# Kernel tuning notes

Hardware: AMD Instinct MI355X
Metric: run time of the kernel (lower is better)

Reference implementation:

```python
import jax, jax.numpy as jnp
import numpy as np


def setup_inputs() -> dict:
    key = jax.random.key(0)
    k1, k2 = jax.random.split(key)
    N, P, SMK, L = 256, 64, 2048, 32
    inp = jax.random.normal(k1, (N, P, SMK, 2), dtype=jnp.float32)
    # channel taps; in the original these are randn scaled by sqrt(power/2)
    cof = jax.random.normal(k2, (N, P, L, 2), dtype=jnp.float32) * 0.1
    return {"input": inp, "cof": cof, "M": 64}


def reference(input, cof, M):
    # input: (N, P, SMK, 2) real/imag stacked; cof: (N, P, L, 2)
    N, P, SMK, _ = input.shape
    L = cof.shape[2]
    sig = (input[..., 0] + 1j * input[..., 1]).reshape(N * P, SMK)   # complex64
    h = (cof[..., 0] + 1j * cof[..., 1]).reshape(N * P, L)
    # torch path: conv1d with time-reversed taps and padding=L-1 == FULL linear
    # convolution; four real convs == one complex conv.
    out_c = jax.vmap(lambda s, k: jnp.convolve(s, k, mode="full"))(sig, h)  # (N*P, SMK+L-1)
    output = jnp.stack([out_c.real, out_c.imag], axis=-1).reshape(N, P, SMK + L - 1, 2)
    # H_t = FFT of zero-padded taps along the tap axis (length M)
    cof_zp = jnp.pad(cof, ((0, 0), (0, 0), (0, M - L), (0, 0)))
    Hc = jnp.fft.fft(cof_zp[..., 0] + 1j * cof_zp[..., 1], axis=-1)  # (N, P, M)
    H_t = jnp.stack([Hc.real, Hc.imag], axis=-1)                      # (N, P, M, 2)
    return output, H_t
```

## Files before the change

### kernel.cpp

```cpp
#include <hip/hip_runtime.h>
#include <math.h>

#define SMK    2048
#define TAPS   32
#define OUTLEN (SMK + TAPS - 1)
#define PAD    32
#define SLOTS  (PAD + SMK + PAD)
#define MDFT   64

typedef float v2f __attribute__((ext_vector_type(2)));

__device__ __forceinline__ int swz(int p) { return p ^ ((p >> 4) & 15); }

__device__ __forceinline__ float rfl(float x) {
    return __int_as_float(__builtin_amdgcn_readfirstlane(__float_as_int(x)));
}

__global__ __launch_bounds__(256)
void conv_kernel(const float* __restrict__ input,
                 const float* __restrict__ cof,
                 float* __restrict__ out0,
                 float* __restrict__ out1)
{
    __shared__ float2 s_sig[SLOTS];
    __shared__ float2 s_tw[MDFT];

    const int tid = threadIdx.x;
    const int row = blockIdx.x;

    const float4* gin = (const float4*)(input + (size_t)row * (SMK * 2));
    #pragma unroll
    for (int k = 0; k < 4; ++k) {
        float4 v = gin[tid + 256 * k];
        int i0 = PAD + 2 * (tid + 256 * k);
        s_sig[swz(i0)]     = make_float2(v.x, v.y);
        s_sig[swz(i0 + 1)] = make_float2(v.z, v.w);
    }
    if (tid < PAD) {
        s_sig[swz(tid)] = make_float2(0.f, 0.f);
    } else if (tid < 2 * PAD) {
        s_sig[swz(SMK + tid)] = make_float2(0.f, 0.f);
    }
    if (tid >= 64 && tid < 128) {
        int j = tid - 64;
        float sv, cv;
        __sincosf(-2.0f * (float)M_PI * (float)j / (float)MDFT, &sv, &cv);
        s_tw[j] = make_float2(cv, sv);
    }

    const float2* __restrict__ ct = (const float2*)(cof + (size_t)row * (TAPS * 2));
    float hre[TAPS], him[TAPS];
    #pragma unroll
    for (int l = 0; l < TAPS; ++l) {
        float2 tv = ct[l];
        hre[l] = rfl(tv.x);
        him[l] = rfl(tv.y);
    }
    __syncthreads();

    const int t0 = tid * 8;

    v2f accA[8], accB[8];
    #pragma unroll
    for (int k = 0; k < 8; ++k) { accA[k] = (v2f)(0.f); accB[k] = (v2f)(0.f); }

    #pragma unroll
    for (int c = 0; c < 2; ++c) {
        float2 win[23];
        const int sbase = t0 + 1 + 16 * (1 - c);
        #pragma unroll
        for (int j = 0; j < 23; ++j) win[j] = s_sig[swz(sbase + j)];

        #pragma unroll
        for (int lp = 0; lp < 16; ++lp) {
            const int l = 16 * c + lp;
            const v2f hv = { hre[l], him[l] };
            #pragma unroll
            for (int k = 0; k < 8; ++k) {
                const float2 s = win[k - lp + 15];
                accA[k] = __builtin_elementwise_fma((v2f){ s.x, s.x }, hv, accA[k]);
                accB[k] = __builtin_elementwise_fma((v2f){ s.y, s.y }, hv, accB[k]);
            }
        }
        __builtin_amdgcn_sched_barrier(0);
    }

    float2* go2 = (float2*)(out0 + (size_t)row * (OUTLEN * 2));
    #pragma unroll
    for (int k = 0; k < 8; ++k)
        go2[t0 + k] = make_float2(accA[k].x - accB[k].y, accA[k].y + accB[k].x);

    if (tid < MDFT) {
        const int kk = tid;
        v2f aA = (v2f)(0.f), aB = (v2f)(0.f);
        #pragma unroll
        for (int l = 0; l < TAPS; ++l) {
            const v2f hv = { hre[l], him[l] };
            float2 w = s_tw[(kk * l) & (MDFT - 1)];
            aA = __builtin_elementwise_fma((v2f){ w.x, w.x }, hv, aA);
            aB = __builtin_elementwise_fma((v2f){ w.y, w.y }, hv, aB);
        }
        ((float2*)out1)[(size_t)row * MDFT + kk] =
            make_float2(aA.x - aB.y, aA.y + aB.x);
    }
    else if (tid >= 128 && tid < 128 + (OUTLEN - SMK)) {
        const int t = SMK + (tid - 128);
        v2f aA = (v2f)(0.f), aB = (v2f)(0.f);
        #pragma unroll
        for (int l = 0; l < TAPS; ++l) {
            const v2f hv = { hre[l], him[l] };
            float2 s = s_sig[swz(PAD + t - l)];
            aA = __builtin_elementwise_fma((v2f){ s.x, s.x }, hv, aA);
            aB = __builtin_elementwise_fma((v2f){ s.y, s.y }, hv, aB);
        }
        go2[t] = make_float2(aA.x - aB.y, aA.y + aB.x);
    }
}

extern "C" void kernel_launch(void* const* d_in, const int* in_sizes, int n_in,
                              void* d_out, int out_size, void* d_ws, size_t ws_size,
                              hipStream_t stream)
{
    const float* input = (const float*)d_in[0];
    const float* cof   = (const float*)d_in[1];

    const int NP = in_sizes[0] / (SMK * 2);

    float* out0 = (float*)d_out;
    float* out1 = out0 + (size_t)NP * OUTLEN * 2;

    conv_kernel<<<NP, 256, 0, stream>>>(input, cof, out0, out1);
}
```

Before: 146.2 us.

## Use unswizzled float4 LDS layout with 4-output register tiles per pass

Drops the XOR-swizzled float2 shared buffer in favour of a plain float4 array, so the global-to-LDS copy is a direct 128-bit store and the window reads are wide float4 loads. The conv work is split into two passes of 4 outputs per thread, each over 4 tap chunks of 8, with outputs shifted by one so the tail threads also cover output 0. Launch bounds now request 8 blocks per CU to cut register pressure and raise occupancy. In exchange there is more LDS traffic per output from the smaller tiles, possible bank conflicts without the swizzle, and less ILP per thread.

```diff
diff --git a/kernel.cpp b/kernel.cpp
--- a/kernel.cpp
+++ b/kernel.cpp
@@ -6,23 +6,22 @@
 #define OUTLEN (SMK + TAPS - 1)
 #define PAD    32
 #define SLOTS  (PAD + SMK + PAD)
+#define NF4    (SLOTS / 2)
 #define MDFT   64
 
 typedef float v2f __attribute__((ext_vector_type(2)));
-
-__device__ __forceinline__ int swz(int p) { return p ^ ((p >> 4) & 15); }
 
 __device__ __forceinline__ float rfl(float x) {
     return __int_as_float(__builtin_amdgcn_readfirstlane(__float_as_int(x)));
 }
 
-__global__ __launch_bounds__(256)
+__global__ __launch_bounds__(256, 8)
 void conv_kernel(const float* __restrict__ input,
                  const float* __restrict__ cof,
                  float* __restrict__ out0,
                  float* __restrict__ out1)
 {
-    __shared__ float2 s_sig[SLOTS];
+    __shared__ float4 S4[NF4];
     __shared__ float2 s_tw[MDFT];
 
     const int tid = threadIdx.x;
@@ -30,16 +29,11 @@
 
     const float4* gin = (const float4*)(input + (size_t)row * (SMK * 2));
     #pragma unroll
-    for (int k = 0; k < 4; ++k) {
-        float4 v = gin[tid + 256 * k];
-        int i0 = PAD + 2 * (tid + 256 * k);
-        s_sig[swz(i0)]     = make_float2(v.x, v.y);
-        s_sig[swz(i0 + 1)] = make_float2(v.z, v.w);
-    }
-    if (tid < PAD) {
-        s_sig[swz(tid)] = make_float2(0.f, 0.f);
-    } else if (tid < 2 * PAD) {
-        s_sig[swz(SMK + tid)] = make_float2(0.f, 0.f);
+    for (int k = 0; k < 4; ++k) S4[16 + tid + 256 * k] = gin[tid + 256 * k];
+    if (tid < 16) {
+        S4[tid] = make_float4(0.f, 0.f, 0.f, 0.f);
+    } else if (tid < 32) {
+        S4[1024 + tid] = make_float4(0.f, 0.f, 0.f, 0.f);
     }
     if (tid >= 64 && tid < 128) {
         int j = tid - 64;
@@ -58,37 +52,45 @@
     }
     __syncthreads();
 
-    const int t0 = tid * 8;
+    float2* go2 = (float2*)(out0 + (size_t)row * (OUTLEN * 2));
 
-    v2f accA[8], accB[8];
-    #pragma unroll
-    for (int k = 0; k < 8; ++k) { accA[k] = (v2f)(0.f); accB[k] = (v2f)(0.f); }
+    #pragma unroll 1
+    for (int j = 0; j < 2; ++j) {
+        const int tf = 4 * tid + 1 + 1024 * j;
 
-    #pragma unroll
-    for (int c = 0; c < 2; ++c) {
-        float2 win[23];
-        const int sbase = t0 + 1 + 16 * (1 - c);
+        v2f accA[4], accB[4];
         #pragma unroll
-        for (int j = 0; j < 23; ++j) win[j] = s_sig[swz(sbase + j)];
+        for (int k = 0; k < 4; ++k) { accA[k] = (v2f)(0.f); accB[k] = (v2f)(0.f); }
 
         #pragma unroll
-        for (int lp = 0; lp < 16; ++lp) {
-            const int l = 16 * c + lp;
-            const v2f hv = { hre[l], him[l] };
+        for (int c = 0; c < 4; ++c) {
+            const int base4 = 2 * tid + 512 * j - 4 * c + 13;
+            float4 w4[6];
             #pragma unroll
-            for (int k = 0; k < 8; ++k) {
-                const float2 s = win[k - lp + 15];
-                accA[k] = __builtin_elementwise_fma((v2f){ s.x, s.x }, hv, accA[k]);
-                accB[k] = __builtin_elementwise_fma((v2f){ s.y, s.y }, hv, accB[k]);
+            for (int i = 0; i < 6; ++i) w4[i] = S4[base4 + i];
+
+            #pragma unroll
+            for (int lp = 0; lp < 8; ++lp) {
+                const int l = 8 * c + lp;
+                const v2f hv = { hre[l], him[l] };
+                #pragma unroll
+                for (int k = 0; k < 4; ++k) {
+                    const int q = k - lp + 7;
+                    const float sx = (q & 1) ? w4[q >> 1].z : w4[q >> 1].x;
+                    const float sy = (q & 1) ? w4[q >> 1].w : w4[q >> 1].y;
+                    accA[k] = __builtin_elementwise_fma((v2f){ sx, sx }, hv, accA[k]);
+                    accB[k] = __builtin_elementwise_fma((v2f){ sy, sy }, hv, accB[k]);
+                }
             }
+            __builtin_amdgcn_sched_barrier(0);
         }
-        __builtin_amdgcn_sched_barrier(0);
+
+        #pragma unroll
+        for (int k = 0; k < 4; ++k)
+            go2[tf + k] = make_float2(accA[k].x - accB[k].y, accA[k].y + accB[k].x);
     }
 
-    float2* go2 = (float2*)(out0 + (size_t)row * (OUTLEN * 2));
-    #pragma unroll
-    for (int k = 0; k < 8; ++k)
-        go2[t0 + k] = make_float2(accA[k].x - accB[k].y, accA[k].y + accB[k].x);
+    const float2* S2 = (const float2*)S4;
 
     if (tid < MDFT) {
         const int kk = tid;
@@ -103,13 +105,13 @@
         ((float2*)out1)[(size_t)row * MDFT + kk] =
             make_float2(aA.x - aB.y, aA.y + aB.x);
     }
-    else if (tid >= 128 && tid < 128 + (OUTLEN - SMK)) {
-        const int t = SMK + (tid - 128);
+    else if (tid >= 128 && tid <= 158) {
+        const int t = (tid == 158) ? 0 : (2049 + (tid - 128));
         v2f aA = (v2f)(0.f), aB = (v2f)(0.f);
         #pragma unroll
         for (int l = 0; l < TAPS; ++l) {
             const v2f hv = { hre[l], him[l] };
-            float2 s = s_sig[swz(PAD + t - l)];
+            float2 s = S2[PAD + t - l];
             aA = __builtin_elementwise_fma((v2f){ s.x, s.x }, hv, aA);
             aB = __builtin_elementwise_fma((v2f){ s.y, s.y }, hv, aB);
         }
```

After: 139.7 us. 1.05x faster.
